# Optimization experiments

Hardware: AMD Instinct MI355X
Metric: run time of the kernel (lower is better)

The kernel has to match this reference:

```python
import jax, jax.numpy as jnp
import numpy as np

N = 100000
D = 256
E = 1600000
H, C = 2, 32  # heads, out_channels


def setup_inputs() -> dict:
    key = jax.random.key(0)
    ks = jax.random.split(key, 10)
    h_x = jax.random.normal(ks[0], (N, D), dtype=jnp.float32)
    t_x = jax.random.normal(ks[1], (N, D), dtype=jnp.float32)
    src = jax.random.randint(ks[2], (E,), 0, N, dtype=jnp.int32)
    off = jax.random.randint(ks[3], (E,), 1, N, dtype=jnp.int32)
    dst = (src + off) % N  # guarantees src != dst (remove_self_loops is a no-op)
    edge_index = jnp.stack([src, dst])  # [2, E]
    enrichment_weights = jax.random.uniform(ks[4], (E,), dtype=jnp.float32) * 3.0
    s = 1.0 / np.sqrt(D)
    W_src = jax.random.normal(ks[5], (D, H * C), dtype=jnp.float32) * s
    W_dst = jax.random.normal(ks[6], (D, H * C), dtype=jnp.float32) * s
    att_src = jax.random.normal(ks[7], (H, C), dtype=jnp.float32) * 0.1
    att_dst = jax.random.normal(ks[8], (H, C), dtype=jnp.float32) * 0.1
    bias = jnp.zeros((H * C,), dtype=jnp.float32)
    enrichment_scale = jnp.float32(0.5)
    return {"h_x": h_x, "t_x": t_x, "edge_index": edge_index,
            "enrichment_weights": enrichment_weights,
            "W_src": W_src, "W_dst": W_dst, "att_src": att_src,
            "att_dst": att_dst, "bias": bias,
            "enrichment_scale": enrichment_scale}


def _gat(x_src, x_dst, src, dst, num_dst, W_src, W_dst, att_src, att_dst, bias):
    # PyG GATConv, bipartite, heads=H, out=C, concat=True, eval mode
    hs = (x_src @ W_src).reshape(-1, H, C)  # [Ns, H, C]
    hd = (x_dst @ W_dst).reshape(-1, H, C)  # [Nd, H, C]
    a_s = jnp.einsum('nhc,hc->nh', hs, att_src)  # [Ns, H]
    a_d = jnp.einsum('nhc,hc->nh', hd, att_dst)  # [Nd, H]
    alpha = jax.nn.leaky_relu(a_s[src] + a_d[dst], 0.2)  # [E', H]
    m = jax.ops.segment_max(alpha, dst, num_segments=num_dst)
    alpha = jnp.exp(alpha - m[dst])
    z = jax.ops.segment_sum(alpha, dst, num_segments=num_dst)
    alpha = alpha / (z[dst] + 1e-16)
    msg = hs[src] * alpha[:, :, None]  # [E', H, C]
    out = jax.ops.segment_sum(msg, dst, num_segments=num_dst)  # [Nd, H, C]
    return out.reshape(num_dst, H * C) + bias


def reference(h_x, t_x, edge_index, enrichment_weights,
              W_src, W_dst, att_src, att_dst, bias, enrichment_scale):
    h_in = jax.nn.elu(h_x)
    t_in = jax.nn.elu(t_x)
    src, dst = edge_index[0], edge_index[1]
    loops = jnp.arange(min(h_x.shape[0], t_x.shape[0]), dtype=src.dtype)
    # direction 1: (h -> t), PyG appends self-loops after the input edges
    s1 = jnp.concatenate([src, loops]); d1 = jnp.concatenate([dst, loops])
    t_rep = _gat(h_in, t_in, s1, d1, t_x.shape[0], W_src, W_dst, att_src, att_dst, bias)
    # direction 2: reversed edges (t -> h)
    s2 = jnp.concatenate([dst, loops]); d2 = jnp.concatenate([src, loops])
    h_rep = _gat(t_in, h_in, s2, d2, h_x.shape[0], W_src, W_dst, att_src, att_dst, bias)
    # edge-enrichment reweighting (scalar factor)
    scale = 0.5 * jnp.tanh(enrichment_scale)
    ew = jnp.clip(enrichment_weights, 0.3, 3.0)
    aw = jax.nn.softmax(ew)
    weighted = jnp.sum(aw * ew)
    factor = 1.0 + scale * (weighted - 1.0)
    return (h_rep * factor, t_rep * factor)
```

## Files before the change

kernel.cpp:

```cpp
#include <hip/hip_runtime.h>
#include <hip/hip_fp16.h>
#include <math.h>

typedef __attribute__((ext_vector_type(8))) short bf16x8;
typedef __attribute__((ext_vector_type(4))) float f32x4;

__device__ __forceinline__ float bf2f(unsigned short u) {
    union { unsigned int i; float f; } c;
    c.i = ((unsigned int)u) << 16;
    return c.f;
}
__device__ __forceinline__ unsigned short f2bf(float f) {
    union { float f; unsigned int i; } c;
    c.f = f;
    unsigned int b = c.i + 0x7FFFu + ((c.i >> 16) & 1u);
    return (unsigned short)(b >> 16);
}
__device__ __forceinline__ float eluf(float v) {
    return v > 0.f ? v : (__expf(v) - 1.f);
}
__device__ __forceinline__ float lrelu(float v) {
    return v >= 0.f ? v : 0.2f * v;
}
__device__ __forceinline__ unsigned int fenc(float f) {
    union { float f; unsigned int u; } c; c.f = f;
    return (c.u & 0x80000000u) ? ~c.u : (c.u | 0x80000000u);
}
__device__ __forceinline__ float fdec(unsigned int k) {
    union { float f; unsigned int u; } c;
    c.u = (k & 0x80000000u) ? (k ^ 0x80000000u) : ~k;
    return c.f;
}

__global__ void detect_kernel(const unsigned int* __restrict__ w, int nwords,
                              int* __restrict__ flag)
{
    __shared__ int cnt_s;
    if (threadIdx.x == 0) cnt_s = 0;
    __syncthreads();
    int sane = 0;
    for (int i = threadIdx.x; i < nwords; i += 256) {
        unsigned int lo = w[i] & 0xffffu;
        int e = (int)((lo >> 7) & 0xffu);
        if (e >= 114 && e <= 136) sane++;
    }
    atomicAdd(&cnt_s, sane);
    __syncthreads();
    if (threadIdx.x == 0) *flag = (2 * cnt_s > nwords) ? 1 : 0;
}

__global__ __launch_bounds__(256) void wfrag_kernel(
    const void* __restrict__ Wsrc, const void* __restrict__ Wdst,
    const int* __restrict__ flag,
    unsigned short* __restrict__ Whi, unsigned short* __restrict__ Wlo)
{
    const int isbf = *flag;
    const int nch = 8 * 8 * 64;
    for (int ch = blockIdx.x * 256 + threadIdx.x; ch < nch; ch += gridDim.x * 256) {
        int l  = ch & 63;
        int t  = (ch >> 6) & 7;
        int ks = ch >> 9;
        int col = t * 16 + (l & 15);
        int k0  = ks * 32 + (l >> 4) * 8;
        if (isbf) {
            const unsigned short* W = (col < 64)
                ? ((const unsigned short*)Wsrc + col)
                : ((const unsigned short*)Wdst + (col - 64));
#pragma unroll
            for (int j = 0; j < 8; ++j) {
                Whi[(size_t)ch * 8 + j] = W[(size_t)(k0 + j) * 64];
                Wlo[(size_t)ch * 8 + j] = 0;
            }
        } else {
            const float* W = (col < 64)
                ? ((const float*)Wsrc + col)
                : ((const float*)Wdst + (col - 64));
#pragma unroll
            for (int j = 0; j < 8; ++j) {
                float wv = W[(size_t)(k0 + j) * 64];
                unsigned short h = f2bf(wv);
                Whi[(size_t)ch * 8 + j] = h;
                Wlo[(size_t)ch * 8 + j] = f2bf(wv - bf2f(h));
            }
        }
    }
}

__global__ __launch_bounds__(256) void gemm_fused_kernel(
    const void* __restrict__ xh, const void* __restrict__ xt,
    const unsigned short* __restrict__ Whi, const unsigned short* __restrict__ Wlo,
    const void* __restrict__ att_src, const void* __restrict__ att_dst,
    const int* __restrict__ flag,
    __half* __restrict__ P, float* __restrict__ as_all, float* __restrict__ ad_all,
    int N)
{
    const int isbf = *flag;
    __half* Pout = P + (size_t)blockIdx.y * (size_t)N * 64u;
    float* asO  = as_all + (size_t)blockIdx.y * (size_t)N * 2u;
    float* adO  = ad_all + (size_t)blockIdx.y * (size_t)N * 2u;
    const int tid = threadIdx.x;
    const int w   = tid >> 6;
    const int l   = tid & 63;
    const int l15 = l & 15;
    const int lhi = l >> 4;
    const int rowA = blockIdx.x * 64 + w * 16 + l15;
    const bool rv = rowA < N;

    bf16x8 ahi[8], alo[8];
    if (isbf) {
        const unsigned short* xv = (const unsigned short*)((blockIdx.y == 0) ? xh : xt);
#pragma unroll
        for (int ks = 0; ks < 8; ++ks) {
            union { bf16x8 v; unsigned int u[4]; } o;
            if (rv) {
                uint4 raw = *(const uint4*)(xv + (size_t)rowA * 256 + ks * 32 + lhi * 8);
                unsigned int wsr[4] = {raw.x, raw.y, raw.z, raw.w};
#pragma unroll
                for (int i = 0; i < 4; ++i) {
                    float lo = eluf(bf2f((unsigned short)(wsr[i] & 0xffffu)));
                    float hi = eluf(bf2f((unsigned short)(wsr[i] >> 16)));
                    o.u[i] = (unsigned int)f2bf(lo) | ((unsigned int)f2bf(hi) << 16);
                }
            } else {
                o.u[0] = o.u[1] = o.u[2] = o.u[3] = 0u;
            }
            ahi[ks] = o.v;
            alo[ks] = o.v;
        }
    } else {
        const float* xv = (const float*)((blockIdx.y == 0) ? xh : xt);
#pragma unroll
        for (int ks = 0; ks < 8; ++ks) {
            union { bf16x8 v; unsigned int u[4]; } oh, ol;
            if (rv) {
                const float4* px = (const float4*)(xv + (size_t)rowA * 256 + ks * 32 + lhi * 8);
                float4 f0 = px[0], f1 = px[1];
                float v[8] = {f0.x, f0.y, f0.z, f0.w, f1.x, f1.y, f1.z, f1.w};
#pragma unroll
                for (int i = 0; i < 8; ++i) v[i] = eluf(v[i]);
#pragma unroll
                for (int i = 0; i < 4; ++i) {
                    unsigned short h0 = f2bf(v[2 * i]);
                    unsigned short h1 = f2bf(v[2 * i + 1]);
                    unsigned short l0 = f2bf(v[2 * i]     - bf2f(h0));
                    unsigned short l1 = f2bf(v[2 * i + 1] - bf2f(h1));
                    oh.u[i] = (unsigned int)h0 | ((unsigned int)h1 << 16);
                    ol.u[i] = (unsigned int)l0 | ((unsigned int)l1 << 16);
                }
            } else {
                oh.u[0] = oh.u[1] = oh.u[2] = oh.u[3] = 0u;
                ol.u[0] = ol.u[1] = ol.u[2] = ol.u[3] = 0u;
            }
            ahi[ks] = oh.v;
            alo[ks] = ol.v;
        }
    }

    f32x4 acc[8];
#pragma unroll
    for (int t = 0; t < 8; ++t) acc[t] = (f32x4){0.f, 0.f, 0.f, 0.f};

    const bf16x8* wfh = (const bf16x8*)Whi;
    const bf16x8* wfl = (const bf16x8*)Wlo;
    if (isbf) {
#pragma unroll
        for (int ks = 0; ks < 8; ++ks) {
#pragma unroll
            for (int t = 0; t < 8; ++t) {
                bf16x8 b = wfh[(ks * 8 + t) * 64 + l];
                acc[t] = __builtin_amdgcn_mfma_f32_16x16x32_bf16(ahi[ks], b, acc[t], 0, 0, 0);
            }
        }
    } else {
#pragma unroll
        for (int ks = 0; ks < 8; ++ks) {
#pragma unroll
            for (int t = 0; t < 8; ++t) {
                bf16x8 bh = wfh[(ks * 8 + t) * 64 + l];
                bf16x8 bl = wfl[(ks * 8 + t) * 64 + l];
                acc[t] = __builtin_amdgcn_mfma_f32_16x16x32_bf16(ahi[ks], bh, acc[t], 0, 0, 0);
                acc[t] = __builtin_amdgcn_mfma_f32_16x16x32_bf16(alo[ks], bh, acc[t], 0, 0, 0);
                acc[t] = __builtin_amdgcn_mfma_f32_16x16x32_bf16(ahi[ks], bl, acc[t], 0, 0, 0);
            }
        }
    }

    float asv[4], adv[4];
#pragma unroll
    for (int t = 0; t < 4; ++t) {
        if (isbf) {
            asv[t] = bf2f(((const unsigned short*)att_src)[t * 16 + l15]);
            adv[t] = bf2f(((const unsigned short*)att_dst)[t * 16 + l15]);
        } else {
            asv[t] = ((const float*)att_src)[t * 16 + l15];
            adv[t] = ((const float*)att_dst)[t * 16 + l15];
        }
    }
    const int rbase = blockIdx.x * 64 + w * 16 + lhi * 4;
#pragma unroll
    for (int reg = 0; reg < 4; ++reg) {
        int row = rbase + reg;
        bool ok = row < N;
        if (ok) {
            __half* p = Pout + (size_t)row * 64 + l15;
#pragma unroll
            for (int t = 0; t < 4; ++t) p[t * 16] = __float2half(acc[t][reg]);
        }
        float s0 = acc[0][reg] * asv[0] + acc[1][reg] * asv[1];
        float s1 = acc[2][reg] * asv[2] + acc[3][reg] * asv[3];
        float d0 = acc[4][reg] * adv[0] + acc[5][reg] * adv[1];
        float d1 = acc[6][reg] * adv[2] + acc[7][reg] * adv[3];
#pragma unroll
        for (int o2 = 8; o2 >= 1; o2 >>= 1) {
            s0 += __shfl_xor(s0, o2, 64);
            s1 += __shfl_xor(s1, o2, 64);
            d0 += __shfl_xor(d0, o2, 64);
            d1 += __shfl_xor(d1, o2, 64);
        }
        if (ok && l15 == 0) {
            asO[(size_t)row * 2 + 0] = s0;
            asO[(size_t)row * 2 + 1] = s1;
            adO[(size_t)row * 2 + 0] = d0;
            adO[(size_t)row * 2 + 1] = d1;
        }
    }
}

__global__ __launch_bounds__(256) void gemm_elu_kernel(
    const void* __restrict__ xh, const void* __restrict__ xt,
    const void* __restrict__ Wsrc, const void* __restrict__ Wdst,
    const void* __restrict__ att_src, const void* __restrict__ att_dst,
    const int* __restrict__ flag,
    __half* __restrict__ P, float* __restrict__ as_all, float* __restrict__ ad_all,
    int N, int D)
{
    const int isbf = *flag;
    __shared__ float xs[64][33];
    __shared__ float wt[32][128];
    const void* xv = (blockIdx.y == 0) ? xh : xt;
    __half* Pout = P + (size_t)blockIdx.y * (size_t)N * 64u;
    float* asO  = as_all + (size_t)blockIdx.y * (size_t)N * 2u;
    float* adO  = ad_all + (size_t)blockIdx.y * (size_t)N * 2u;
    const int rowBase = blockIdx.x * 64;
    const int tid = threadIdx.x;
    const int tcx = tid & 15;
    const int tcy = tid >> 4;

    float acc[4][8];
#pragma unroll
    for (int r = 0; r < 4; ++r)
#pragma unroll
        for (int c = 0; c < 8; ++c) acc[r][c] = 0.f;

    for (int kc = 0; kc < D; kc += 32) {
        {
            int row = tid >> 2;
            int kq  = (tid & 3) * 8;
            int r = rowBase + row;
            float v[8];
            if (r < N) {
                if (isbf) {
                    const unsigned short* xb = (const unsigned short*)xv;
                    uint4 raw = *(const uint4*)(xb + (size_t)r * D + kc + kq);
                    unsigned int ws[4] = {raw.x, raw.y, raw.z, raw.w};
#pragma unroll
                    for (int i = 0; i < 4; ++i) {
                        v[2 * i]     = bf2f((unsigned short)(ws[i] & 0xffffu));
                        v[2 * i + 1] = bf2f((unsigned short)(ws[i] >> 16));
                    }
                } else {
                    const float* xf = (const float*)xv;
                    const float4* p4 = (const float4*)(xf + (size_t)r * D + kc + kq);
                    float4 f0 = p4[0], f1 = p4[1];
                    v[0] = f0.x; v[1] = f0.y; v[2] = f0.z; v[3] = f0.w;
                    v[4] = f1.x; v[5] = f1.y; v[6] = f1.z; v[7] = f1.w;
                }
#pragma unroll
                for (int i = 0; i < 8; ++i) v[i] = eluf(v[i]);
            } else {
#pragma unroll
                for (int i = 0; i < 8; ++i) v[i] = 0.f;
            }
#pragma unroll
            for (int i = 0; i < 8; ++i) xs[row][kq + i] = v[i];
        }
#pragma unroll
        for (int i = 0; i < 2; ++i) {
            int f = (tid + i * 256) * 8;
            int k = f >> 7;
            int c = f & 127;
            float v[8];
            if (isbf) {
                const unsigned short* Wp = (c < 64)
                    ? ((const unsigned short*)Wsrc + (size_t)(kc + k) * 64 + c)
                    : ((const unsigned short*)Wdst + (size_t)(kc + k) * 64 + (c - 64));
                uint4 raw = *(const uint4*)Wp;
                unsigned int ws[4] = {raw.x, raw.y, raw.z, raw.w};
#pragma unroll
                for (int q = 0; q < 4; ++q) {
                    v[2 * q]     = bf2f((unsigned short)(ws[q] & 0xffffu));
                    v[2 * q + 1] = bf2f((unsigned short)(ws[q] >> 16));
                }
            } else {
                const float* Wp = (c < 64)
                    ? ((const float*)Wsrc + (size_t)(kc + k) * 64 + c)
                    : ((const float*)Wdst + (size_t)(kc + k) * 64 + (c - 64));
                const float4* p4 = (const float4*)Wp;
                float4 f0 = p4[0], f1 = p4[1];
                v[0] = f0.x; v[1] = f0.y; v[2] = f0.z; v[3] = f0.w;
                v[4] = f1.x; v[5] = f1.y; v[6] = f1.z; v[7] = f1.w;
            }
#pragma unroll
            for (int q = 0; q < 8; ++q) wt[k][c + q] = v[q];
        }
        __syncthreads();
#pragma unroll 8
        for (int k = 0; k < 32; ++k) {
            float xr[4];
#pragma unroll
            for (int r = 0; r < 4; ++r) xr[r] = xs[tcy * 4 + r][k];
            float4 w0 = *(const float4*)&wt[k][tcx * 8];
            float4 w1 = *(const float4*)&wt[k][tcx * 8 + 4];
#pragma unroll
            for (int r = 0; r < 4; ++r) {
                acc[r][0] += xr[r] * w0.x; acc[r][1] += xr[r] * w0.y;
                acc[r][2] += xr[r] * w0.z; acc[r][3] += xr[r] * w0.w;
                acc[r][4] += xr[r] * w1.x; acc[r][5] += xr[r] * w1.y;
                acc[r][6] += xr[r] * w1.z; acc[r][7] += xr[r] * w1.w;
            }
        }
        __syncthreads();
    }

    float attv[8];
#pragma unroll
    for (int q = 0; q < 8; ++q) {
        int c = tcx * 8 + q;
        if (isbf) attv[q] = (c < 64) ? bf2f(((const unsigned short*)att_src)[c])
                                     : bf2f(((const unsigned short*)att_dst)[c - 64]);
        else      attv[q] = (c < 64) ? ((const float*)att_src)[c]
                                     : ((const float*)att_dst)[c - 64];
    }

#pragma unroll
    for (int r = 0; r < 4; ++r) {
        int row = rowBase + tcy * 4 + r;
        bool ok = row < N;
        if (ok && tcx < 8) {
            __half* p = Pout + (size_t)row * 64 + tcx * 8;
#pragma unroll
            for (int q = 0; q < 8; ++q) p[q] = __float2half(acc[r][q]);
        }
        float part = 0.f;
#pragma unroll
        for (int q = 0; q < 8; ++q) part += acc[r][q] * attv[q];
        part += __shfl_xor(part, 1, 64);
        part += __shfl_xor(part, 2, 64);
        if (ok && (tcx & 3) == 0) {
            if (tcx == 0)       asO[(size_t)row * 2 + 0] = part;
            else if (tcx == 4)  asO[(size_t)row * 2 + 1] = part;
            else if (tcx == 8)  adO[(size_t)row * 2 + 0] = part;
            else                adO[(size_t)row * 2 + 1] = part;
        }
    }
}

__global__ __launch_bounds__(256) void gmax_kernel(
    const float* __restrict__ as_all, unsigned int* __restrict__ gmax, int N)
{
    unsigned int k0 = 0, k1 = 0, k2 = 0, k3 = 0;
    const int total = 2 * N;
    for (int i = blockIdx.x * 256 + threadIdx.x; i < total; i += gridDim.x * 256) {
        float2 v = *(const float2*)(as_all + (size_t)i * 2);
        unsigned int ex = fenc(v.x), ey = fenc(v.y);
        if (i < N) { k0 = max(k0, ex); k1 = max(k1, ey); }
        else       { k2 = max(k2, ex); k3 = max(k3, ey); }
    }
#pragma unroll
    for (int o = 32; o >= 1; o >>= 1) {
        k0 = max(k0, (unsigned int)__shfl_xor((int)k0, o, 64));
        k1 = max(k1, (unsigned int)__shfl_xor((int)k1, o, 64));
        k2 = max(k2, (unsigned int)__shfl_xor((int)k2, o, 64));
        k3 = max(k3, (unsigned int)__shfl_xor((int)k3, o, 64));
    }
    if ((threadIdx.x & 63) == 0) {
        atomicMax(&gmax[0], k0);
        atomicMax(&gmax[1], k1);
        atomicMax(&gmax[2], k2);
        atomicMax(&gmax[3], k3);
    }
}

__global__ void count_kernel(const int* __restrict__ srce, const int* __restrict__ dste,
                             int* __restrict__ cnt, int N, int E)
{
    int e = blockIdx.x * blockDim.x + threadIdx.x;
    if (e >= E) return;
    atomicAdd(&cnt[dste[e]], 1);
    atomicAdd(&cnt[N + srce[e]], 1);
}

__global__ __launch_bounds__(256) void scan_bsum_kernel(
    const int* __restrict__ cnt, int M, int chunk, int* __restrict__ bsum)
{
    __shared__ int r[4];
    int beg = blockIdx.x * chunk;
    int end = beg + chunk; if (end > M) end = M;
    int s = 0;
    for (int i = beg + threadIdx.x; i < end; i += 256) s += cnt[i];
#pragma unroll
    for (int o = 32; o >= 1; o >>= 1) s += __shfl_down(s, o, 64);
    int lane = threadIdx.x & 63, wv = threadIdx.x >> 6;
    if (lane == 0) r[wv] = s;
    __syncthreads();
    if (threadIdx.x == 0) bsum[blockIdx.x] = r[0] + r[1] + r[2] + r[3];
}

__global__ __launch_bounds__(256) void scan_boff_kernel(
    const int* __restrict__ bsum, int NB, int* __restrict__ boff)
{
    __shared__ int s[256];
    int t = threadIdx.x;
    int v = (t < NB) ? bsum[t] : 0;
    s[t] = v;
    __syncthreads();
    for (int o = 1; o < 256; o <<= 1) {
        int x = (t >= o) ? s[t - o] : 0;
        __syncthreads();
        s[t] += x;
        __syncthreads();
    }
    if (t < NB) boff[t] = s[t] - v;
}

__global__ __launch_bounds__(256) void scan_write_kernel(
    const int* __restrict__ cnt, int M, int chunk,
    const int* __restrict__ boff, int* __restrict__ off)
{
    __shared__ int s[256];
    int t = threadIdx.x;
    int beg = blockIdx.x * chunk;
    int end = beg + chunk; if (end > M) end = M;
    if (beg >= M) return;
    int running = boff[blockIdx.x];
    for (int base = beg; base < end; base += 256) {
        int i = base + t;
        int v = (i < end) ? cnt[i] : 0;
        s[t] = v;
        __syncthreads();
        for (int o = 1; o < 256; o <<= 1) {
            int x = (t >= o) ? s[t - o] : 0;
            __syncthreads();
            s[t] += x;
            __syncthreads();
        }
        if (i < end) off[i] = running + s[t] - v;
        int total = s[255];
        __syncthreads();
        running += total;
    }
    if (end == M && t == 0) off[M] = running;
}

__global__ void fill_kernel(const int* __restrict__ srce, const int* __restrict__ dste,
                            const int* __restrict__ off, int* __restrict__ cur,
                            int* __restrict__ idx, int N, int E)
{
    int e = blockIdx.x * blockDim.x + threadIdx.x;
    if (e >= E) return;
    int s = srce[e], d = dste[e];
    int p  = atomicAdd(&cur[d], 1);
    idx[off[d] + p] = s;
    int p2 = atomicAdd(&cur[N + s], 1);
    idx[off[N + s] + p2] = d;
}

__global__ __launch_bounds__(256) void enrich_kernel(
    const void* __restrict__ ew, const int* __restrict__ flag,
    float* __restrict__ S, int E)
{
    __shared__ float r1[4], r2[4];
    const int isbf = *flag;
    float e1 = 0.f, e2 = 0.f;
    for (int i = blockIdx.x * 256 + threadIdx.x; i < E; i += gridDim.x * 256) {
        float c = isbf ? bf2f(((const unsigned short*)ew)[i]) : ((const float*)ew)[i];
        c = fminf(fmaxf(c, 0.3f), 3.0f);
        float ex = __expf(c);
        e1 += ex;
        e2 += c * ex;
    }
#pragma unroll
    for (int o = 32; o >= 1; o >>= 1) {
        e1 += __shfl_down(e1, o, 64);
        e2 += __shfl_down(e2, o, 64);
    }
    int lane = threadIdx.x & 63;
    int wv = threadIdx.x >> 6;
    if (lane == 0) { r1[wv] = e1; r2[wv] = e2; }
    __syncthreads();
    if (threadIdx.x == 0) {
        atomicAdd(&S[0], r1[0] + r1[1] + r1[2] + r1[3]);
        atomicAdd(&S[1], r2[0] + r2[1] + r2[2] + r2[3]);
    }
}

__global__ __launch_bounds__(256) void agg_kernel(
    const int* __restrict__ off, const int* __restrict__ idx,
    const float* __restrict__ as_all, const float* __restrict__ ad_all,
    const __half* __restrict__ Pall,
    const void* __restrict__ bias,
    const float* __restrict__ S,
    const unsigned int* __restrict__ gmax,
    const void* __restrict__ esc,
    const int* __restrict__ flag,
    void* __restrict__ out, int N)
{
    const int isbf = *flag;
    int q = (blockIdx.x * 256 + threadIdx.x) >> 6;
    int lane = threadIdx.x & 63;
    if (q >= 2 * N) return;
    int dir = (q >= N) ? 1 : 0;
    int n = q - dir * N;
    const float* a_s  = as_all + (size_t)dir * 2u * (size_t)N;
    const float* a_d  = ad_all + (size_t)(1 - dir) * 2u * (size_t)N;
    const __half* Psrc = Pall + (size_t)dir * (size_t)N * 64u;
    size_t outOff = dir ? 0u : (size_t)N * 64u;
    const int hi = lane >> 5;
    const int jb = off[q], je = off[q + 1];

    float2 adv2 = *(const float2*)(a_d + (size_t)n * 2);
    const float adv = hi ? adv2.y : adv2.x;
    const float gm  = fdec(gmax[dir * 2 + hi]);
    const float m   = lrelu(gm + adv);

    float2 ass2 = *(const float2*)(a_s + (size_t)n * 2);
    const float pSelf = __expf(lrelu((hi ? ass2.y : ass2.x) + adv) - m);
    float z0 = pSelf, z1 = 0.f;
    float acc0 = pSelf * __half2float(Psrc[(size_t)n * 64 + lane]);
    float acc1 = 0.f;

    int j = jb;
    for (; j + 1 < je; j += 2) {
        int s0 = idx[j], s1 = idx[j + 1];
        float2 a0 = *(const float2*)(a_s + (size_t)s0 * 2);
        float2 a1 = *(const float2*)(a_s + (size_t)s1 * 2);
        float h0 = __half2float(Psrc[(size_t)s0 * 64 + lane]);
        float h1 = __half2float(Psrc[(size_t)s1 * 64 + lane]);
        float p0 = __expf(lrelu((hi ? a0.y : a0.x) + adv) - m);
        float p1 = __expf(lrelu((hi ? a1.y : a1.x) + adv) - m);
        z0 += p0; acc0 = fmaf(p0, h0, acc0);
        z1 += p1; acc1 = fmaf(p1, h1, acc1);
    }
    if (j < je) {
        int s0 = idx[j];
        float2 a0 = *(const float2*)(a_s + (size_t)s0 * 2);
        float h0 = __half2float(Psrc[(size_t)s0 * 64 + lane]);
        float p0 = __expf(lrelu((hi ? a0.y : a0.x) + adv) - m);
        z0 += p0; acc0 = fmaf(p0, h0, acc0);
    }
    float z   = z0 + z1;
    float acc = acc0 + acc1;

    float escv = isbf ? bf2f(((const unsigned short*)esc)[0]) : ((const float*)esc)[0];
    float bv   = isbf ? bf2f(((const unsigned short*)bias)[lane]) : ((const float*)bias)[lane];
    float weighted = S[1] / S[0];
    float factor = 1.f + 0.5f * tanhf(escv) * (weighted - 1.f);
    float o = (acc / (z + 1e-16f) + bv) * factor;
    size_t oi = outOff + (size_t)n * 64 + lane;
    if (isbf) ((unsigned short*)out)[oi] = f2bf(o);
    else      ((float*)out)[oi] = o;
}

extern "C" void kernel_launch(void* const* d_in, const int* in_sizes, int n_in,
                              void* d_out, int out_size, void* d_ws, size_t ws_size,
                              hipStream_t stream)
{
    const void* hx      = d_in[0];
    const void* tx      = d_in[1];
    const int*  eidx    = (const int*)d_in[2];
    const void* ew      = d_in[3];
    const void* Wsrc    = d_in[4];
    const void* Wdst    = d_in[5];
    const void* att_src = d_in[6];
    const void* att_dst = d_in[7];
    const void* bias    = d_in[8];
    const void* esc     = d_in[9];

    const int HC = in_sizes[6];
    const int D  = in_sizes[4] / HC;
    const int N  = in_sizes[0] / D;
    const int E  = in_sizes[3];
    const int* srce = eidx;
    const int* dste = eidx + E;

    const bool canM = (D == 256) && (HC == 64);

    char* wsb = (char*)d_ws;
    size_t o = 0;
    auto alloc = [&](size_t bytes) -> void* {
        void* p = wsb + o;
        o += (bytes + 255) & ~(size_t)255;
        return p;
    };
    __half* Pall  = (__half*)alloc((size_t)2 * N * 64 * 2);
    float* as_all = (float*)alloc((size_t)2 * N * 2 * 4);
    float* ad_all = (float*)alloc((size_t)2 * N * 2 * 4);
    float* S      = (float*)alloc(2 * 4);
    unsigned int* gmax = (unsigned int*)alloc(4 * 4);
    int*   cnt    = (int*)alloc((size_t)2 * N * 4);
    int*   offp   = (int*)alloc(((size_t)2 * N + 1) * 4);
    int*   cur    = (int*)alloc((size_t)2 * N * 4);
    int*   idx    = (int*)alloc((size_t)2 * E * 4);
    int*   flag   = (int*)alloc(256);
    int*   bsum   = (int*)alloc(256 * 4);
    int*   boff   = (int*)alloc(256 * 4);
    unsigned short* Whi = (unsigned short*)alloc((size_t)8 * 8 * 64 * 8 * 2);
    unsigned short* Wlo = (unsigned short*)alloc((size_t)8 * 8 * 64 * 8 * 2);

    hipMemsetAsync(cnt, 0, (size_t)2 * N * 4, stream);
    hipMemsetAsync(cur, 0, (size_t)2 * N * 4, stream);
    hipMemsetAsync(S, 0, 2 * 4, stream);
    hipMemsetAsync(gmax, 0, 4 * 4, stream);

    detect_kernel<<<1, 256, 0, stream>>>((const unsigned int*)hx, 65536, flag);

    dim3 gGemm((N + 63) / 64, 2);
    if (canM) {
        wfrag_kernel<<<16, 256, 0, stream>>>(Wsrc, Wdst, flag, Whi, Wlo);
        gemm_fused_kernel<<<gGemm, 256, 0, stream>>>(hx, tx, Whi, Wlo,
                                                     att_src, att_dst, flag,
                                                     Pall, as_all, ad_all, N);
    } else {
        gemm_elu_kernel<<<gGemm, 256, 0, stream>>>(hx, tx, Wsrc, Wdst, att_src, att_dst,
                                                   flag, Pall, as_all, ad_all, N, D);
    }
    gmax_kernel<<<256, 256, 0, stream>>>(as_all, gmax, N);
    count_kernel<<<(E + 255) / 256, 256, 0, stream>>>(srce, dste, cnt, N, E);

    const int M = 2 * N;
    int chunk = (M + 255) / 256;
    chunk = (chunk + 255) & ~255;
    const int NB = (M + chunk - 1) / chunk;
    scan_bsum_kernel<<<NB, 256, 0, stream>>>(cnt, M, chunk, bsum);
    scan_boff_kernel<<<1, 256, 0, stream>>>(bsum, NB, boff);
    scan_write_kernel<<<NB, 256, 0, stream>>>(cnt, M, chunk, boff, offp);

    fill_kernel<<<(E + 255) / 256, 256, 0, stream>>>(srce, dste, offp, cur, idx, N, E);
    enrich_kernel<<<512, 256, 0, stream>>>(ew, flag, S, E);

    agg_kernel<<<(2 * N + 3) / 4, 256, 0, stream>>>(offp, idx, as_all, ad_all,
                                                    Pall, bias, S, gmax, esc, flag,
                                                    d_out, N);
}
```

Baseline: 960.0 us.

## Precompute per-edge softmax weights in CSR fill and pack with neighbor index

The per-edge attention exponentials are now computed once in the fill kernel, which runs per edge, and stored next to the neighbor index in a 16-byte packed CSR entry. This removes the 64-lane redundant gather of attention scalars and the exp from the aggregation loop. Attention scores are also merged into one float4 per node. The aggregation loop is unrolled by 4 with separate accumulators. The cost is four times the edge-array footprint, written with scattered 16-byte stores, and each lane now reads 16 bytes per edge instead of 4.

```diff
diff --git a/kernel.cpp b/kernel.cpp
--- a/kernel.cpp
+++ b/kernel.cpp
@@ -91,13 +91,11 @@
     const unsigned short* __restrict__ Whi, const unsigned short* __restrict__ Wlo,
     const void* __restrict__ att_src, const void* __restrict__ att_dst,
     const int* __restrict__ flag,
-    __half* __restrict__ P, float* __restrict__ as_all, float* __restrict__ ad_all,
-    int N)
+    __half* __restrict__ P, float4* __restrict__ av, int N)
 {
     const int isbf = *flag;
     __half* Pout = P + (size_t)blockIdx.y * (size_t)N * 64u;
-    float* asO  = as_all + (size_t)blockIdx.y * (size_t)N * 2u;
-    float* adO  = ad_all + (size_t)blockIdx.y * (size_t)N * 2u;
+    float4* avO  = av + (size_t)blockIdx.y * (size_t)N;
     const int tid = threadIdx.x;
     const int w   = tid >> 6;
     const int l   = tid & 63;
@@ -217,12 +215,7 @@
             d0 += __shfl_xor(d0, o2, 64);
             d1 += __shfl_xor(d1, o2, 64);
         }
-        if (ok && l15 == 0) {
-            asO[(size_t)row * 2 + 0] = s0;
-            asO[(size_t)row * 2 + 1] = s1;
-            adO[(size_t)row * 2 + 0] = d0;
-            adO[(size_t)row * 2 + 1] = d1;
-        }
+        if (ok && l15 == 0) avO[row] = make_float4(s0, s1, d0, d1);
     }
 }
 
@@ -231,16 +224,14 @@
     const void* __restrict__ Wsrc, const void* __restrict__ Wdst,
     const void* __restrict__ att_src, const void* __restrict__ att_dst,
     const int* __restrict__ flag,
-    __half* __restrict__ P, float* __restrict__ as_all, float* __restrict__ ad_all,
-    int N, int D)
+    __half* __restrict__ P, float4* __restrict__ av, int N, int D)
 {
     const int isbf = *flag;
     __shared__ float xs[64][33];
     __shared__ float wt[32][128];
     const void* xv = (blockIdx.y == 0) ? xh : xt;
     __half* Pout = P + (size_t)blockIdx.y * (size_t)N * 64u;
-    float* asO  = as_all + (size_t)blockIdx.y * (size_t)N * 2u;
-    float* adO  = ad_all + (size_t)blockIdx.y * (size_t)N * 2u;
+    float4* avO  = av + (size_t)blockIdx.y * (size_t)N;
     const int rowBase = blockIdx.x * 64;
     const int tid = threadIdx.x;
     const int tcx = tid & 15;
@@ -356,22 +347,18 @@
         for (int q = 0; q < 8; ++q) part += acc[r][q] * attv[q];
         part += __shfl_xor(part, 1, 64);
         part += __shfl_xor(part, 2, 64);
-        if (ok && (tcx & 3) == 0) {
-            if (tcx == 0)       asO[(size_t)row * 2 + 0] = part;
-            else if (tcx == 4)  asO[(size_t)row * 2 + 1] = part;
-            else if (tcx == 8)  adO[(size_t)row * 2 + 0] = part;
-            else                adO[(size_t)row * 2 + 1] = part;
-        }
+        if (ok && (tcx & 3) == 0)
+            ((float*)&avO[row])[tcx >> 2] = part;
     }
 }
 
 __global__ __launch_bounds__(256) void gmax_kernel(
-    const float* __restrict__ as_all, unsigned int* __restrict__ gmax, int N)
+    const float4* __restrict__ av, unsigned int* __restrict__ gmax, int N)
 {
     unsigned int k0 = 0, k1 = 0, k2 = 0, k3 = 0;
     const int total = 2 * N;
     for (int i = blockIdx.x * 256 + threadIdx.x; i < total; i += gridDim.x * 256) {
-        float2 v = *(const float2*)(as_all + (size_t)i * 2);
+        float4 v = av[i];
         unsigned int ex = fenc(v.x), ey = fenc(v.y);
         if (i < N) { k0 = max(k0, ex); k1 = max(k1, ey); }
         else       { k2 = max(k2, ex); k3 = max(k3, ey); }
@@ -464,15 +451,25 @@
 
 __global__ void fill_kernel(const int* __restrict__ srce, const int* __restrict__ dste,
                             const int* __restrict__ off, int* __restrict__ cur,
-                            int* __restrict__ idx, int N, int E)
+                            const float4* __restrict__ av,
+                            const unsigned int* __restrict__ gmax,
+                            int4* __restrict__ epack, int N, int E)
 {
     int e = blockIdx.x * blockDim.x + threadIdx.x;
     if (e >= E) return;
     int s = srce[e], d = dste[e];
+    float4 ah = av[s];
+    float4 at = av[N + d];
+    float gm00 = fdec(gmax[0]), gm01 = fdec(gmax[1]);
+    float gm10 = fdec(gmax[2]), gm11 = fdec(gmax[3]);
+    float p00 = __expf(lrelu(ah.x + at.z) - lrelu(gm00 + at.z));
+    float p01 = __expf(lrelu(ah.y + at.w) - lrelu(gm01 + at.w));
+    float p10 = __expf(lrelu(at.x + ah.z) - lrelu(gm10 + ah.z));
+    float p11 = __expf(lrelu(at.y + ah.w) - lrelu(gm11 + ah.w));
     int p  = atomicAdd(&cur[d], 1);
-    idx[off[d] + p] = s;
+    epack[off[d] + p] = make_int4(s, __float_as_int(p00), __float_as_int(p01), 0);
     int p2 = atomicAdd(&cur[N + s], 1);
-    idx[off[N + s] + p2] = d;
+    epack[off[N + s] + p2] = make_int4(d, __float_as_int(p10), __float_as_int(p11), 0);
 }
 
 __global__ __launch_bounds__(256) void enrich_kernel(
@@ -505,9 +502,8 @@
 }
 
 __global__ __launch_bounds__(256) void agg_kernel(
-    const int* __restrict__ off, const int* __restrict__ idx,
-    const float* __restrict__ as_all, const float* __restrict__ ad_all,
-    const __half* __restrict__ Pall,
+    const int* __restrict__ off, const int4* __restrict__ epack,
+    const float4* __restrict__ av, const __half* __restrict__ Pall,
     const void* __restrict__ bias,
     const float* __restrict__ S,
     const unsigned int* __restrict__ gmax,
@@ -521,45 +517,45 @@
     if (q >= 2 * N) return;
     int dir = (q >= N) ? 1 : 0;
     int n = q - dir * N;
-    const float* a_s  = as_all + (size_t)dir * 2u * (size_t)N;
-    const float* a_d  = ad_all + (size_t)(1 - dir) * 2u * (size_t)N;
     const __half* Psrc = Pall + (size_t)dir * (size_t)N * 64u;
     size_t outOff = dir ? 0u : (size_t)N * 64u;
     const int hi = lane >> 5;
     const int jb = off[q], je = off[q + 1];
 
-    float2 adv2 = *(const float2*)(a_d + (size_t)n * 2);
-    const float adv = hi ? adv2.y : adv2.x;
-    const float gm  = fdec(gmax[dir * 2 + hi]);
-    const float m   = lrelu(gm + adv);
-
-    float2 ass2 = *(const float2*)(a_s + (size_t)n * 2);
-    const float pSelf = __expf(lrelu((hi ? ass2.y : ass2.x) + adv) - m);
-    float z0 = pSelf, z1 = 0.f;
-    float acc0 = pSelf * __half2float(Psrc[(size_t)n * 64 + lane]);
-    float acc1 = 0.f;
+    float4 asrc = av[(size_t)dir * N + n];
+    float4 adst = av[(size_t)(1 - dir) * N + n];
+    const float adv = hi ? adst.w : adst.z;
+    const float m   = lrelu(fdec(gmax[dir * 2 + hi]) + adv);
+    const float pSelf = __expf(lrelu((hi ? asrc.y : asrc.x) + adv) - m);
+
+    float z0 = pSelf, z1 = 0.f, z2 = 0.f, z3 = 0.f;
+    float a0 = pSelf * __half2float(Psrc[(size_t)n * 64 + lane]);
+    float a1 = 0.f, a2 = 0.f, a3 = 0.f;
 
     int j = jb;
-    for (; j + 1 < je; j += 2) {
-        int s0 = idx[j], s1 = idx[j + 1];
-        float2 a0 = *(const float2*)(a_s + (size_t)s0 * 2);
-        float2 a1 = *(const float2*)(a_s + (size_t)s1 * 2);
-        float h0 = __half2float(Psrc[(size_t)s0 * 64 + lane]);
-        float h1 = __half2float(Psrc[(size_t)s1 * 64 + lane]);
-        float p0 = __expf(lrelu((hi ? a0.y : a0.x) + adv) - m);
-        float p1 = __expf(lrelu((hi ? a1.y : a1.x) + adv) - m);
-        z0 += p0; acc0 = fmaf(p0, h0, acc0);
-        z1 += p1; acc1 = fmaf(p1, h1, acc1);
-    }
-    if (j < je) {
-        int s0 = idx[j];
-        float2 a0 = *(const float2*)(a_s + (size_t)s0 * 2);
-        float h0 = __half2float(Psrc[(size_t)s0 * 64 + lane]);
-        float p0 = __expf(lrelu((hi ? a0.y : a0.x) + adv) - m);
-        z0 += p0; acc0 = fmaf(p0, h0, acc0);
-    }
-    float z   = z0 + z1;
-    float acc = acc0 + acc1;
+    for (; j + 3 < je; j += 4) {
+        int4 e0 = epack[j], e1 = epack[j + 1], e2 = epack[j + 2], e3 = epack[j + 3];
+        float h0 = __half2float(Psrc[(size_t)e0.x * 64 + lane]);
+        float h1 = __half2float(Psrc[(size_t)e1.x * 64 + lane]);
+        float h2 = __half2float(Psrc[(size_t)e2.x * 64 + lane]);
+        float h3 = __half2float(Psrc[(size_t)e3.x * 64 + lane]);
+        float p0 = __int_as_float(hi ? e0.z : e0.y);
+        float p1 = __int_as_float(hi ? e1.z : e1.y);
+        float p2 = __int_as_float(hi ? e2.z : e2.y);
+        float p3 = __int_as_float(hi ? e3.z : e3.y);
+        z0 += p0; a0 = fmaf(p0, h0, a0);
+        z1 += p1; a1 = fmaf(p1, h1, a1);
+        z2 += p2; a2 = fmaf(p2, h2, a2);
+        z3 += p3; a3 = fmaf(p3, h3, a3);
+    }
+    for (; j < je; ++j) {
+        int4 e0 = epack[j];
+        float h0 = __half2float(Psrc[(size_t)e0.x * 64 + lane]);
+        float p0 = __int_as_float(hi ? e0.z : e0.y);
+        z0 += p0; a0 = fmaf(p0, h0, a0);
+    }
+    float z   = (z0 + z1) + (z2 + z3);
+    float acc = (a0 + a1) + (a2 + a3);
 
     float escv = isbf ? bf2f(((const unsigned short*)esc)[0]) : ((const float*)esc)[0];
     float bv   = isbf ? bf2f(((const unsigned short*)bias)[lane]) : ((const float*)bias)[lane];
@@ -603,14 +599,13 @@
         return p;
     };
     __half* Pall  = (__half*)alloc((size_t)2 * N * 64 * 2);
-    float* as_all = (float*)alloc((size_t)2 * N * 2 * 4);
-    float* ad_all = (float*)alloc((size_t)2 * N * 2 * 4);
+    float4* av    = (float4*)alloc((size_t)2 * N * 16);
     float* S      = (float*)alloc(2 * 4);
     unsigned int* gmax = (unsigned int*)alloc(4 * 4);
     int*   cnt    = (int*)alloc((size_t)2 * N * 4);
     int*   offp   = (int*)alloc(((size_t)2 * N + 1) * 4);
     int*   cur    = (int*)alloc((size_t)2 * N * 4);
-    int*   idx    = (int*)alloc((size_t)2 * E * 4);
+    int4*  epack  = (int4*)alloc((size_t)2 * E * 16);
     int*   flag   = (int*)alloc(256);
     int*   bsum   = (int*)alloc(256 * 4);
     int*   boff   = (int*)alloc(256 * 4);
@@ -629,12 +624,12 @@
         wfrag_kernel<<<16, 256, 0, stream>>>(Wsrc, Wdst, flag, Whi, Wlo);
         gemm_fused_kernel<<<gGemm, 256, 0, stream>>>(hx, tx, Whi, Wlo,
                                                      att_src, att_dst, flag,
-                                                     Pall, as_all, ad_all, N);
+                                                     Pall, av, N);
     } else {
         gemm_elu_kernel<<<gGemm, 256, 0, stream>>>(hx, tx, Wsrc, Wdst, att_src, att_dst,
-                                                   flag, Pall, as_all, ad_all, N, D);
-    }
-    gmax_kernel<<<256, 256, 0, stream>>>(as_all, gmax, N);
+                                                   flag, Pall, av, N, D);
+    }
+    gmax_kernel<<<256, 256, 0, stream>>>(av, gmax, N);
     count_kernel<<<(E + 255) / 256, 256, 0, stream>>>(srce, dste, cnt, N, E);
 
     const int M = 2 * N;
@@ -645,10 +640,11 @@
     scan_boff_kernel<<<1, 256, 0, stream>>>(bsum, NB, boff);
     scan_write_kernel<<<NB, 256, 0, stream>>>(cnt, M, chunk, boff, offp);
 
-    fill_kernel<<<(E + 255) / 256, 256, 0, stream>>>(srce, dste, offp, cur, idx, N, E);
+    fill_kernel<<<(E + 255) / 256, 256, 0, stream>>>(srce, dste, offp, cur,
+                                                     av, gmax, epack, N, E);
     enrich_kernel<<<512, 256, 0, stream>>>(ew, flag, S, E);
 
-    agg_kernel<<<(2 * N + 3) / 4, 256, 0, stream>>>(offp, idx, as_all, ad_all,
+    agg_kernel<<<(2 * N + 3) / 4, 256, 0, stream>>>(offp, epack, av,
                                                     Pall, bias, S, gmax, esc, flag,
                                                     d_out, N);
 }
```

After: 884.0 us. 1.09x faster.
